# Kernel tuning notes

Hardware: AMD Instinct MI355X
Metric: run time of the kernel (lower is better)

Reference implementation:

```python
import jax, jax.numpy as jnp
import numpy as np

D_MODEL = 1024
NUM_HEADS = 16
D_K = D_MODEL // NUM_HEADS
BATCH = 4
SEQ = 2048


def setup_inputs() -> dict:
    key = jax.random.key(0)
    ks = jax.random.split(key, 16)
    s = 0.02
    return {
        "query": jax.random.normal(ks[0], (BATCH, SEQ, D_MODEL), jnp.float32),
        "key": jax.random.normal(ks[1], (BATCH, SEQ, D_MODEL), jnp.float32),
        "value": jax.random.normal(ks[2], (BATCH, SEQ, D_MODEL), jnp.float32),
        "Wq": jax.random.normal(ks[3], (D_MODEL, D_MODEL), jnp.float32) * s,
        "bq": jnp.zeros((D_MODEL,), jnp.float32),
        "Wk": jax.random.normal(ks[4], (D_MODEL, D_MODEL), jnp.float32) * s,
        "bk": jnp.zeros((D_MODEL,), jnp.float32),
        "Wv": jax.random.normal(ks[5], (D_MODEL, D_MODEL), jnp.float32) * s,
        "bv": jnp.zeros((D_MODEL,), jnp.float32),
        "Wo": jax.random.normal(ks[6], (D_MODEL, D_MODEL), jnp.float32) * s,
        "bo": jnp.zeros((D_MODEL,), jnp.float32),
        "gamma": jnp.ones((D_MODEL,), jnp.float32),
        "beta": jnp.zeros((D_MODEL,), jnp.float32),
    }


def _layer_norm(x, gamma, beta, eps=1e-5):
    mu = jnp.mean(x, axis=-1, keepdims=True)
    var = jnp.var(x, axis=-1, keepdims=True)
    return (x - mu) * jax.lax.rsqrt(var + eps) * gamma + beta


def reference(query, key, value, Wq, bq, Wk, bk, Wv, bv, Wo, bo, gamma, beta):
    B, S, _ = query.shape
    residual = query
    # projections -> [B, H, S, d_k]
    Q = (query @ Wq + bq).reshape(B, S, NUM_HEADS, D_K).transpose(0, 2, 1, 3)
    K = (key @ Wk + bk).reshape(B, -1, NUM_HEADS, D_K).transpose(0, 2, 1, 3)
    V = (value @ Wv + bv).reshape(B, -1, NUM_HEADS, D_K).transpose(0, 2, 1, 3)
    scale = 1.0 / jnp.sqrt(jnp.asarray(D_K, query.dtype))
    scores = jnp.einsum("bhqd,bhkd->bhqk", Q, K) * scale  # [B,H,S,S]
    attn = jax.nn.softmax(scores, axis=-1)
    ctx = jnp.einsum("bhqk,bhkd->bhqd", attn, V)
    ctx = ctx.transpose(0, 2, 1, 3).reshape(B, S, D_MODEL)
    out = ctx @ Wo + bo
    return _layer_norm(residual + out, gamma, beta)
```

## Files before the change

kernel.cpp:

```cpp
#include <hip/hip_runtime.h>

#define D_MODEL 1024
#define NUM_HEADS 16
#define DK 64
#define BATCH 4
#define SEQ 2048
#define MTOT (BATCH*SEQ)

typedef __attribute__((ext_vector_type(8))) short short8;
typedef __attribute__((ext_vector_type(4))) float f32x4;

__device__ __forceinline__ unsigned short f2bf(float f) {
    union { float f; unsigned u; } v; v.f = f;
    unsigned r = v.u + 0x7FFFu + ((v.u >> 16) & 1u);
    return (unsigned short)(r >> 16);
}

__device__ __forceinline__ void gload16(const unsigned short* g, unsigned short* l) {
    __builtin_amdgcn_global_load_lds(
        (const __attribute__((address_space(1))) unsigned int*)g,
        (__attribute__((address_space(3))) unsigned int*)l, 16, 0, 0);
}

__global__ __launch_bounds__(256) void mha_wtrans4(
    const float* __restrict__ W0, const float* __restrict__ W1,
    const float* __restrict__ W2, const float* __restrict__ W3,
    unsigned short* __restrict__ T0, unsigned short* __restrict__ T1,
    unsigned short* __restrict__ T2, unsigned short* __restrict__ T3) {
    __shared__ float tile[64][65];
    int z = blockIdx.z;
    const float* W = z == 0 ? W0 : z == 1 ? W1 : z == 2 ? W2 : W3;
    unsigned short* WT = z == 0 ? T0 : z == 1 ? T1 : z == 2 ? T2 : T3;
    int n0 = blockIdx.x * 64, k0 = blockIdx.y * 64;
    int tx = threadIdx.x & 63, ty = threadIdx.x >> 6;
#pragma unroll
    for (int i = 0; i < 16; ++i)
        tile[ty + i * 4][tx] = W[(size_t)(k0 + ty + i * 4) * D_MODEL + n0 + tx];
    __syncthreads();
#pragma unroll
    for (int i = 0; i < 16; ++i)
        WT[(size_t)(n0 + ty + i * 4) * D_MODEL + k0 + tx] = f2bf(tile[tx][ty + i * 4]);
}

__global__ __launch_bounds__(256) void mha_cvt3(
    const float* __restrict__ i0, const float* __restrict__ i1, const float* __restrict__ i2,
    unsigned short* __restrict__ o0, unsigned short* __restrict__ o1, unsigned short* __restrict__ o2) {
    int y = blockIdx.y;
    const float* in = y == 0 ? i0 : y == 1 ? i1 : i2;
    unsigned short* out = y == 0 ? o0 : y == 1 ? o1 : o2;
    int i = blockIdx.x * 256 + threadIdx.x;
    float4 v = reinterpret_cast<const float4*>(in)[i];
    ushort4 o;
    o.x = f2bf(v.x); o.y = f2bf(v.y); o.z = f2bf(v.z); o.w = f2bf(v.w);
    reinterpret_cast<ushort4*>(out)[i] = o;
}

__device__ __forceinline__ void gemm_stage(const unsigned short* Ag, const unsigned short* Bg,
                                           unsigned short* Al, unsigned short* Bl,
                                           int wid, int rsub, int c8, int kk,
                                           int brow, int bcol) {
#pragma unroll
    for (int q = 0; q < 4; ++q) {
        int i = wid * 4 + q;
        int row = i * 8 + rsub;
        int gcol = kk + ((c8 ^ (row & 7)) << 3);
        gload16(Ag + (size_t)(brow + row) * D_MODEL + gcol, Al + i * 512);
        gload16(Bg + (size_t)(bcol + row) * D_MODEL + gcol, Bl + i * 512);
    }
}

__device__ __forceinline__ void gemm_compute(const unsigned short* Al, const unsigned short* Bl,
                                             f32x4 (&acc)[4][4],
                                             int wr, int wc, int l15, int lg, int l7) {
    short8 af[4][2], bf[4][2];
#pragma unroll
    for (int mi = 0; mi < 4; ++mi)
#pragma unroll
        for (int ks = 0; ks < 2; ++ks)
            af[mi][ks] = *reinterpret_cast<const short8*>(
                &Al[(wr * 64 + mi * 16 + l15) * 64 + (((ks * 4 + lg) ^ l7) << 3)]);
#pragma unroll
    for (int ni = 0; ni < 4; ++ni)
#pragma unroll
        for (int ks = 0; ks < 2; ++ks)
            bf[ni][ks] = *reinterpret_cast<const short8*>(
                &Bl[(wc * 64 + ni * 16 + l15) * 64 + (((ks * 4 + lg) ^ l7) << 3)]);
#pragma unroll
    for (int mi = 0; mi < 4; ++mi)
#pragma unroll
        for (int ni = 0; ni < 4; ++ni)
#pragma unroll
            for (int ks = 0; ks < 2; ++ks)
                acc[mi][ni] = __builtin_amdgcn_mfma_f32_16x16x32_bf16(
                    af[mi][ks], bf[ni][ks], acc[mi][ni], 0, 0, 0);
}

__global__ __launch_bounds__(256) void mha_gemm_qkv(
    const unsigned short* __restrict__ Aq, const unsigned short* __restrict__ Ak,
    const unsigned short* __restrict__ Av,
    const unsigned short* __restrict__ Wq, const unsigned short* __restrict__ Wk,
    const unsigned short* __restrict__ Wv,
    const float* __restrict__ bq, const float* __restrict__ bk, const float* __restrict__ bv,
    unsigned short* __restrict__ Qb, unsigned short* __restrict__ Kb,
    unsigned short* __restrict__ VT, float qscale) {
    __shared__ unsigned short SM[32768];
    unsigned short* A0 = SM;
    unsigned short* B0 = SM + 8192;
    unsigned short* A1 = SM + 16384;
    unsigned short* B1 = SM + 24576;

    int z = blockIdx.z;
    const unsigned short* A = z == 0 ? Aq : z == 1 ? Ak : Av;
    const unsigned short* WT = z == 0 ? Wq : z == 1 ? Wk : Wv;
    const float* bias = z == 0 ? bq : z == 1 ? bk : bv;

    int wid = threadIdx.x >> 6;
    int lane = threadIdx.x & 63;
    int wr = wid >> 1, wc = wid & 1;
    int brow = blockIdx.x * 128;
    int bcol = blockIdx.y * 128;
    int l15 = lane & 15, lg = lane >> 4;
    int c8 = lane & 7, rsub = lane >> 3;
    int l7 = l15 & 7;

    f32x4 acc[4][4] = {};
    gemm_stage(A, WT, A0, B0, wid, rsub, c8, 0, brow, bcol);
    __syncthreads();
    for (int kk = 0; kk < D_MODEL; kk += 128) {
        gemm_stage(A, WT, A1, B1, wid, rsub, c8, kk + 64, brow, bcol);
        gemm_compute(A0, B0, acc, wr, wc, l15, lg, l7);
        __syncthreads();
        if (kk + 128 < D_MODEL)
            gemm_stage(A, WT, A0, B0, wid, rsub, c8, kk + 128, brow, bcol);
        gemm_compute(A1, B1, acc, wr, wc, l15, lg, l7);
        __syncthreads();
    }

    if (z < 2) {
        unsigned short* outb = z == 0 ? Qb : Kb;
        float scale = z == 0 ? qscale : 1.0f;
#pragma unroll
        for (int ni = 0; ni < 4; ++ni) {
            int col = bcol + wc * 64 + ni * 16 + l15;
            float bv2 = bias[col];
#pragma unroll
            for (int mi = 0; mi < 4; ++mi)
#pragma unroll
                for (int j = 0; j < 4; ++j) {
                    int row = brow + wr * 64 + mi * 16 + lg * 4 + j;
                    outb[(size_t)row * D_MODEL + col] = f2bf((acc[mi][ni][j] + bv2) * scale);
                }
        }
    } else {
        unsigned short* T = SM;
#pragma unroll
        for (int ni = 0; ni < 4; ++ni) {
            int c = wc * 64 + ni * 16 + l15;
            float bv2 = bias[bcol + c];
#pragma unroll
            for (int mi = 0; mi < 4; ++mi)
#pragma unroll
                for (int j = 0; j < 4; ++j) {
                    int r = wr * 64 + mi * 16 + lg * 4 + j;
                    T[c * 136 + r] = f2bf(acc[mi][ni][j] + bv2);
                }
        }
        __syncthreads();
        int c = threadIdx.x >> 1;
        int rh = (threadIdx.x & 1) * 64;
        int gcol = bcol + c;
        int h = gcol >> 6, d = gcol & 63;
        int b = brow >> 11, s0 = brow & (SEQ - 1);
        unsigned short* dst = VT + ((size_t)((b * 16 + h) * 64 + d)) * SEQ + s0 + rh;
        const unsigned short* src = &T[c * 136 + rh];
#pragma unroll
        for (int i = 0; i < 8; ++i)
            *reinterpret_cast<short8*>(dst + i * 8) =
                *reinterpret_cast<const short8*>(src + i * 8);
    }
}

__global__ __launch_bounds__(256) void mha_gemm_o(const unsigned short* __restrict__ A,
                                                  const unsigned short* __restrict__ WT,
                                                  const float* __restrict__ bias,
                                                  const float* __restrict__ residual,
                                                  float* __restrict__ outf) {
    __shared__ unsigned short SM[32768];
    unsigned short* A0 = SM;
    unsigned short* B0 = SM + 8192;
    unsigned short* A1 = SM + 16384;
    unsigned short* B1 = SM + 24576;

    int wid = threadIdx.x >> 6;
    int lane = threadIdx.x & 63;
    int wr = wid >> 1, wc = wid & 1;
    int brow = blockIdx.x * 128;
    int bcol = blockIdx.y * 128;
    int l15 = lane & 15, lg = lane >> 4;
    int c8 = lane & 7, rsub = lane >> 3;
    int l7 = l15 & 7;

    f32x4 acc[4][4] = {};
    gemm_stage(A, WT, A0, B0, wid, rsub, c8, 0, brow, bcol);
    __syncthreads();
    for (int kk = 0; kk < D_MODEL; kk += 128) {
        gemm_stage(A, WT, A1, B1, wid, rsub, c8, kk + 64, brow, bcol);
        gemm_compute(A0, B0, acc, wr, wc, l15, lg, l7);
        __syncthreads();
        if (kk + 128 < D_MODEL)
            gemm_stage(A, WT, A0, B0, wid, rsub, c8, kk + 128, brow, bcol);
        gemm_compute(A1, B1, acc, wr, wc, l15, lg, l7);
        __syncthreads();
    }
#pragma unroll
    for (int ni = 0; ni < 4; ++ni) {
        int col = bcol + wc * 64 + ni * 16 + l15;
        float bv2 = bias[col];
#pragma unroll
        for (int mi = 0; mi < 4; ++mi)
#pragma unroll
            for (int j = 0; j < 4; ++j) {
                int row = brow + wr * 64 + mi * 16 + lg * 4 + j;
                outf[(size_t)row * D_MODEL + col] =
                    acc[mi][ni][j] + bv2 + residual[(size_t)row * D_MODEL + col];
            }
    }
}

__device__ __forceinline__ void attn_tile(const unsigned short* Kd,
                                          const unsigned short* Vd,
                                          unsigned short* const* pc,
                                          const unsigned short* Pw,
                                          const short8 aq[2][2],
                                          f32x4 (&acc)[2][4],
                                          float (&lsum)[2][4],
                                          int l15, int lg, int l7) {
    f32x4 s[2][4];
#pragma unroll
    for (int t = 0; t < 4; ++t) {
        int krow = (t * 16 + l15) * 64;
        short8 kf0 = *reinterpret_cast<const short8*>(&Kd[krow + ((lg ^ l7) << 3)]);
        short8 kf1 = *reinterpret_cast<const short8*>(&Kd[krow + (((4 + lg) ^ l7) << 3)]);
#pragma unroll
        for (int m = 0; m < 2; ++m) {
            f32x4 z = {};
            z = __builtin_amdgcn_mfma_f32_16x16x32_bf16(aq[m][0], kf0, z, 0, 0, 0);
            z = __builtin_amdgcn_mfma_f32_16x16x32_bf16(aq[m][1], kf1, z, 0, 0, 0);
            s[m][t] = z;
        }
    }
#pragma unroll
    for (int m = 0; m < 2; ++m)
#pragma unroll
        for (int t = 0; t < 4; ++t)
#pragma unroll
            for (int j = 0; j < 4; ++j) {
                float p = __builtin_amdgcn_exp2f(s[m][t][j]);
                lsum[m][j] += p;
                unsigned u = __builtin_bit_cast(unsigned, p);
                pc[(j & 1) | ((t ^ (j >> 1)) << 1)][m * 1024 + j * 64] =
                    (unsigned short)(u >> 16);
            }
    short8 pf[2][2];
#pragma unroll
    for (int m = 0; m < 2; ++m) {
        int prow = (m * 16 + l15) * 64;
#pragma unroll
        for (int ks = 0; ks < 2; ++ks)
            pf[m][ks] = *reinterpret_cast<const short8*>(
                &Pw[prow + (((ks * 4 + lg) ^ l7) << 3)]);
    }
#pragma unroll
    for (int t = 0; t < 4; ++t) {
        int vrow = (t * 16 + l15) * 64;
        short8 vf0 = *reinterpret_cast<const short8*>(&Vd[vrow + ((lg ^ l7) << 3)]);
        short8 vf1 = *reinterpret_cast<const short8*>(&Vd[vrow + (((4 + lg) ^ l7) << 3)]);
#pragma unroll
        for (int m = 0; m < 2; ++m) {
            acc[m][t] = __builtin_amdgcn_mfma_f32_16x16x32_bf16(pf[m][0], vf0, acc[m][t], 0, 0, 0);
            acc[m][t] = __builtin_amdgcn_mfma_f32_16x16x32_bf16(pf[m][1], vf1, acc[m][t], 0, 0, 0);
        }
    }
}

__global__ __launch_bounds__(256) void mha_attn(const unsigned short* __restrict__ Q,
                                                const unsigned short* __restrict__ K,
                                                const unsigned short* __restrict__ VT,
                                                unsigned short* __restrict__ ctx) {
    __shared__ unsigned short K0[64 * 64], V0[64 * 64];
    __shared__ unsigned short K1[64 * 64], V1[64 * 64];
    __shared__ unsigned short P_lds[4][32 * 64];

    int lane = threadIdx.x & 63;
    int w = threadIdx.x >> 6;
    int l15 = lane & 15, lg = lane >> 4;
    int l7 = l15 & 7;
    int c8 = lane & 7, rsub = lane >> 3;

    int id = blockIdx.x + gridDim.x * blockIdx.y;
    int nid = (id & 7) * 128 + (id >> 3);
    int bx = nid & 15;
    int bh = nid >> 4;
    int b = bh >> 4, h = bh & 15;
    int q0 = bx * 128 + w * 32;

    unsigned short* Pw = P_lds[w];
    unsigned short* pc[8];
    {
        unsigned Bl = lg * 256 + l15 + ((lg & 1) << 5);
#pragma unroll
        for (int c = 0; c < 8; ++c) pc[c] = Pw + (Bl ^ (c << 3));
    }

    short8 aq[2][2];
    {
        const unsigned short* Qp = Q + (size_t)(b * SEQ + q0) * D_MODEL + h * DK;
#pragma unroll
        for (int m = 0; m < 2; ++m)
#pragma unroll
            for (int ks = 0; ks < 2; ++ks)
                aq[m][ks] = *reinterpret_cast<const short8*>(
                    Qp + (size_t)(m * 16 + l15) * D_MODEL + ks * 32 + lg * 8);
    }

    f32x4 acc[2][4] = {};
    float lsum[2][4] = {};

    const unsigned short* Kbh = K + (size_t)(b * SEQ) * D_MODEL + h * DK;
    const unsigned short* VTbh = VT + (size_t)bh * DK * SEQ;

    int i0 = w * 2, i1 = w * 2 + 1;
    int row0 = i0 * 8 + rsub, row1 = i1 * 8 + rsub;
    int sw0 = (c8 ^ (row0 & 7)) << 3, sw1 = (c8 ^ (row1 & 7)) << 3;

#define STAGE(Kd, Vd, kb)                                                        \
    do {                                                                         \
        gload16(Kbh + (size_t)((kb) + row0) * D_MODEL + sw0, (Kd) + i0 * 512);   \
        gload16(Kbh + (size_t)((kb) + row1) * D_MODEL + sw1, (Kd) + i1 * 512);   \
        gload16(VTbh + (size_t)row0 * SEQ + (kb) + sw0, (Vd) + i0 * 512);        \
        gload16(VTbh + (size_t)row1 * SEQ + (kb) + sw1, (Vd) + i1 * 512);        \
    } while (0)

    STAGE(K0, V0, 0);
    __syncthreads();

    for (int kb = 0; kb < SEQ; kb += 128) {
        STAGE(K1, V1, kb + 64);
        attn_tile(K0, V0, pc, Pw, aq, acc, lsum, l15, lg, l7);
        __syncthreads();
        if (kb + 128 < SEQ) STAGE(K0, V0, kb + 128);
        attn_tile(K1, V1, pc, Pw, aq, acc, lsum, l15, lg, l7);
        __syncthreads();
    }
#undef STAGE

#pragma unroll
    for (int m = 0; m < 2; ++m)
#pragma unroll
        for (int j = 0; j < 4; ++j) {
            float l = lsum[m][j];
            l += __shfl_xor(l, 1);
            l += __shfl_xor(l, 2);
            l += __shfl_xor(l, 4);
            l += __shfl_xor(l, 8);
            lsum[m][j] = 1.0f / l;
        }
#pragma unroll
    for (int m = 0; m < 2; ++m)
#pragma unroll
        for (int t = 0; t < 4; ++t)
#pragma unroll
            for (int j = 0; j < 4; ++j) {
                int row = q0 + m * 16 + lg * 4 + j;
                ctx[(size_t)(b * SEQ + row) * D_MODEL + h * DK + t * 16 + l15] =
                    f2bf(acc[m][t][j] * lsum[m][j]);
            }
}

__global__ __launch_bounds__(256) void mha_ln(const float* __restrict__ X,
                                              const float* __restrict__ gamma,
                                              const float* __restrict__ beta,
                                              float* __restrict__ out) {
    int row = blockIdx.x;
    int t = threadIdx.x;
    const float* x = X + (size_t)row * D_MODEL;
    float4 v = reinterpret_cast<const float4*>(x)[t];
    float s = v.x + v.y + v.z + v.w;
    float s2 = v.x * v.x + v.y * v.y + v.z * v.z + v.w * v.w;
#pragma unroll
    for (int off = 1; off < 64; off <<= 1) {
        s += __shfl_xor(s, off);
        s2 += __shfl_xor(s2, off);
    }
    __shared__ float ws[8];
    int wid = t >> 6;
    if ((t & 63) == 0) { ws[wid] = s; ws[4 + wid] = s2; }
    __syncthreads();
    s = ws[0] + ws[1] + ws[2] + ws[3];
    s2 = ws[4] + ws[5] + ws[6] + ws[7];
    float mu = s * (1.f / D_MODEL);
    float var = s2 * (1.f / D_MODEL) - mu * mu;
    float rstd = rsqrtf(var + 1e-5f);
    float4 gv = reinterpret_cast<const float4*>(gamma)[t];
    float4 bv = reinterpret_cast<const float4*>(beta)[t];
    float4 o;
    o.x = (v.x - mu) * rstd * gv.x + bv.x;
    o.y = (v.y - mu) * rstd * gv.y + bv.y;
    o.z = (v.z - mu) * rstd * gv.z + bv.z;
    o.w = (v.w - mu) * rstd * gv.w + bv.w;
    reinterpret_cast<float4*>(out + (size_t)row * D_MODEL)[t] = o;
}

extern "C" void kernel_launch(void* const* d_in, const int* in_sizes, int n_in,
                              void* d_out, int out_size, void* d_ws, size_t ws_size,
                              hipStream_t stream) {
    const float* query = (const float*)d_in[0];
    const float* key   = (const float*)d_in[1];
    const float* value = (const float*)d_in[2];
    const float* Wq = (const float*)d_in[3];
    const float* bq = (const float*)d_in[4];
    const float* Wk = (const float*)d_in[5];
    const float* bk = (const float*)d_in[6];
    const float* Wv = (const float*)d_in[7];
    const float* bv = (const float*)d_in[8];
    const float* Wo = (const float*)d_in[9];
    const float* bo = (const float*)d_in[10];
    const float* gamma = (const float*)d_in[11];
    const float* beta  = (const float*)d_in[12];

    char* ws = (char*)d_ws;
    const size_t MB = 1u << 20;
    unsigned short* WTq = (unsigned short*)(ws + 0 * MB);
    unsigned short* WTk = (unsigned short*)(ws + 2 * MB);
    unsigned short* WTv = (unsigned short*)(ws + 4 * MB);
    unsigned short* WTo = (unsigned short*)(ws + 6 * MB);
    unsigned short* Aq  = (unsigned short*)(ws + 8 * MB);
    unsigned short* Ak  = (unsigned short*)(ws + 24 * MB);
    unsigned short* Av  = (unsigned short*)(ws + 40 * MB);
    unsigned short* Qb  = (unsigned short*)(ws + 56 * MB);
    unsigned short* Kb  = (unsigned short*)(ws + 72 * MB);
    unsigned short* VT  = (unsigned short*)(ws + 88 * MB);
    unsigned short* ctx = (unsigned short*)(ws + 92 * MB);
    float* tmp          = (float*)(ws + 24 * MB);

    const float C1 = 0.180336880f;

    dim3 b256(256);
    mha_wtrans4<<<dim3(16, 16, 4), b256, 0, stream>>>(Wq, Wk, Wv, Wo, WTq, WTk, WTv, WTo);

    int nblk = (MTOT * D_MODEL / 4) / 256;
    mha_cvt3<<<dim3(nblk, 3), b256, 0, stream>>>(query, key, value, Aq, Ak, Av);

    mha_gemm_qkv<<<dim3(MTOT / 128, D_MODEL / 128, 3), b256, 0, stream>>>(
        Aq, Ak, Av, WTq, WTk, WTv, bq, bk, bv, Qb, Kb, VT, C1);

    mha_attn<<<dim3(SEQ / 128, BATCH * NUM_HEADS), b256, 0, stream>>>(Qb, Kb, VT, ctx);

    mha_gemm_o<<<dim3(MTOT / 128, D_MODEL / 128), b256, 0, stream>>>(ctx, WTo, bo, query, tmp);

    mha_ln<<<dim3(MTOT), b256, 0, stream>>>(tmp, gamma, beta, (float*)d_out);
}
```

Baseline: 230.6 us.

## Keep attention probabilities in registers by computing transposed scores

Swaps the MFMA operand order so S^T is computed, letting the exp'd probabilities be packed straight into bf16 B-operand fragments with v_cvt_pk_bf16_f32 instead of round-tripping through a per-wave LDS P buffer. The K rows loaded into LDS are permuted so the accumulator layout matches the operand layout expected by the PV MFMA. Row sums now need only two cross-lane shuffles, output stores become 8-byte vectors, and the removal of the P buffer plus launch_bounds(256,4) aims for higher occupancy. P is now rounded to bf16 (round-to-nearest) rather than truncated, and the row permutation must be exactly right for correctness.

```diff
diff --git a/kernel.cpp b/kernel.cpp
--- a/kernel.cpp
+++ b/kernel.cpp
@@ -9,11 +9,18 @@
 
 typedef __attribute__((ext_vector_type(8))) short short8;
 typedef __attribute__((ext_vector_type(4))) float f32x4;
+typedef __attribute__((ext_vector_type(4))) unsigned int u32x4;
 
 __device__ __forceinline__ unsigned short f2bf(float f) {
     union { float f; unsigned u; } v; v.f = f;
     unsigned r = v.u + 0x7FFFu + ((v.u >> 16) & 1u);
     return (unsigned short)(r >> 16);
+}
+
+__device__ __forceinline__ unsigned cvtpk(float lo, float hi) {
+    unsigned r;
+    asm("v_cvt_pk_bf16_f32 %0, %1, %2" : "=v"(r) : "v"(lo), "v"(hi));
+    return r;
 }
 
 __device__ __forceinline__ void gload16(const unsigned short* g, unsigned short* l) {
@@ -229,13 +236,11 @@
 
 __device__ __forceinline__ void attn_tile(const unsigned short* Kd,
                                           const unsigned short* Vd,
-                                          unsigned short* const* pc,
-                                          const unsigned short* Pw,
                                           const short8 aq[2][2],
                                           f32x4 (&acc)[2][4],
-                                          float (&lsum)[2][4],
+                                          float (&lsum)[2],
                                           int l15, int lg, int l7) {
-    f32x4 s[2][4];
+    f32x4 z[2][4];
 #pragma unroll
     for (int t = 0; t < 4; ++t) {
         int krow = (t * 16 + l15) * 64;
@@ -243,10 +248,10 @@
         short8 kf1 = *reinterpret_cast<const short8*>(&Kd[krow + (((4 + lg) ^ l7) << 3)]);
 #pragma unroll
         for (int m = 0; m < 2; ++m) {
-            f32x4 z = {};
-            z = __builtin_amdgcn_mfma_f32_16x16x32_bf16(aq[m][0], kf0, z, 0, 0, 0);
-            z = __builtin_amdgcn_mfma_f32_16x16x32_bf16(aq[m][1], kf1, z, 0, 0, 0);
-            s[m][t] = z;
+            f32x4 zz = {};
+            zz = __builtin_amdgcn_mfma_f32_16x16x32_bf16(kf0, aq[m][0], zz, 0, 0, 0);
+            zz = __builtin_amdgcn_mfma_f32_16x16x32_bf16(kf1, aq[m][1], zz, 0, 0, 0);
+            z[m][t] = zz;
         }
     }
 #pragma unroll
@@ -255,41 +260,41 @@
         for (int t = 0; t < 4; ++t)
 #pragma unroll
             for (int j = 0; j < 4; ++j) {
-                float p = __builtin_amdgcn_exp2f(s[m][t][j]);
-                lsum[m][j] += p;
-                unsigned u = __builtin_bit_cast(unsigned, p);
-                pc[(j & 1) | ((t ^ (j >> 1)) << 1)][m * 1024 + j * 64] =
-                    (unsigned short)(u >> 16);
+                float p = __builtin_amdgcn_exp2f(z[m][t][j]);
+                z[m][t][j] = p;
+                lsum[m] += p;
             }
     short8 pf[2][2];
 #pragma unroll
-    for (int m = 0; m < 2; ++m) {
-        int prow = (m * 16 + l15) * 64;
-#pragma unroll
-        for (int ks = 0; ks < 2; ++ks)
-            pf[m][ks] = *reinterpret_cast<const short8*>(
-                &Pw[prow + (((ks * 4 + lg) ^ l7) << 3)]);
-    }
-#pragma unroll
-    for (int t = 0; t < 4; ++t) {
-        int vrow = (t * 16 + l15) * 64;
+    for (int m = 0; m < 2; ++m)
+#pragma unroll
+        for (int ks = 0; ks < 2; ++ks) {
+            union { u32x4 u; short8 s; } cv;
+            cv.u = (u32x4){cvtpk(z[m][2 * ks][0], z[m][2 * ks][1]),
+                           cvtpk(z[m][2 * ks][2], z[m][2 * ks][3]),
+                           cvtpk(z[m][2 * ks + 1][0], z[m][2 * ks + 1][1]),
+                           cvtpk(z[m][2 * ks + 1][2], z[m][2 * ks + 1][3])};
+            pf[m][ks] = cv.s;
+        }
+#pragma unroll
+    for (int dt = 0; dt < 4; ++dt) {
+        int vrow = (dt * 16 + l15) * 64;
         short8 vf0 = *reinterpret_cast<const short8*>(&Vd[vrow + ((lg ^ l7) << 3)]);
         short8 vf1 = *reinterpret_cast<const short8*>(&Vd[vrow + (((4 + lg) ^ l7) << 3)]);
 #pragma unroll
         for (int m = 0; m < 2; ++m) {
-            acc[m][t] = __builtin_amdgcn_mfma_f32_16x16x32_bf16(pf[m][0], vf0, acc[m][t], 0, 0, 0);
-            acc[m][t] = __builtin_amdgcn_mfma_f32_16x16x32_bf16(pf[m][1], vf1, acc[m][t], 0, 0, 0);
-        }
-    }
-}
-
-__global__ __launch_bounds__(256) void mha_attn(const unsigned short* __restrict__ Q,
-                                                const unsigned short* __restrict__ K,
-                                                const unsigned short* __restrict__ VT,
-                                                unsigned short* __restrict__ ctx) {
+            acc[m][dt] = __builtin_amdgcn_mfma_f32_16x16x32_bf16(vf0, pf[m][0], acc[m][dt], 0, 0, 0);
+            acc[m][dt] = __builtin_amdgcn_mfma_f32_16x16x32_bf16(vf1, pf[m][1], acc[m][dt], 0, 0, 0);
+        }
+    }
+}
+
+__global__ __launch_bounds__(256, 4) void mha_attn(const unsigned short* __restrict__ Q,
+                                                   const unsigned short* __restrict__ K,
+                                                   const unsigned short* __restrict__ VT,
+                                                   unsigned short* __restrict__ ctx) {
     __shared__ unsigned short K0[64 * 64], V0[64 * 64];
     __shared__ unsigned short K1[64 * 64], V1[64 * 64];
-    __shared__ unsigned short P_lds[4][32 * 64];
 
     int lane = threadIdx.x & 63;
     int w = threadIdx.x >> 6;
@@ -304,14 +309,6 @@
     int b = bh >> 4, h = bh & 15;
     int q0 = bx * 128 + w * 32;
 
-    unsigned short* Pw = P_lds[w];
-    unsigned short* pc[8];
-    {
-        unsigned Bl = lg * 256 + l15 + ((lg & 1) << 5);
-#pragma unroll
-        for (int c = 0; c < 8; ++c) pc[c] = Pw + (Bl ^ (c << 3));
-    }
-
     short8 aq[2][2];
     {
         const unsigned short* Qp = Q + (size_t)(b * SEQ + q0) * D_MODEL + h * DK;
@@ -324,7 +321,7 @@
     }
 
     f32x4 acc[2][4] = {};
-    float lsum[2][4] = {};
+    float lsum[2] = {};
 
     const unsigned short* Kbh = K + (size_t)(b * SEQ) * D_MODEL + h * DK;
     const unsigned short* VTbh = VT + (size_t)bh * DK * SEQ;
@@ -332,11 +329,13 @@
     int i0 = w * 2, i1 = w * 2 + 1;
     int row0 = i0 * 8 + rsub, row1 = i1 * 8 + rsub;
     int sw0 = (c8 ^ (row0 & 7)) << 3, sw1 = (c8 ^ (row1 & 7)) << 3;
+    int sr0 = (row0 & 32) | ((row0 & 12) << 1) | ((row0 & 16) >> 2) | (row0 & 3);
+    int sr1 = (row1 & 32) | ((row1 & 12) << 1) | ((row1 & 16) >> 2) | (row1 & 3);
 
 #define STAGE(Kd, Vd, kb)                                                        \
     do {                                                                         \
-        gload16(Kbh + (size_t)((kb) + row0) * D_MODEL + sw0, (Kd) + i0 * 512);   \
-        gload16(Kbh + (size_t)((kb) + row1) * D_MODEL + sw1, (Kd) + i1 * 512);   \
+        gload16(Kbh + (size_t)((kb) + sr0) * D_MODEL + sw0, (Kd) + i0 * 512);    \
+        gload16(Kbh + (size_t)((kb) + sr1) * D_MODEL + sw1, (Kd) + i1 * 512);    \
         gload16(VTbh + (size_t)row0 * SEQ + (kb) + sw0, (Vd) + i0 * 512);        \
         gload16(VTbh + (size_t)row1 * SEQ + (kb) + sw1, (Vd) + i1 * 512);        \
     } while (0)
@@ -346,35 +345,32 @@
 
     for (int kb = 0; kb < SEQ; kb += 128) {
         STAGE(K1, V1, kb + 64);
-        attn_tile(K0, V0, pc, Pw, aq, acc, lsum, l15, lg, l7);
+        attn_tile(K0, V0, aq, acc, lsum, l15, lg, l7);
         __syncthreads();
         if (kb + 128 < SEQ) STAGE(K0, V0, kb + 128);
-        attn_tile(K1, V1, pc, Pw, aq, acc, lsum, l15, lg, l7);
+        attn_tile(K1, V1, aq, acc, lsum, l15, lg, l7);
         __syncthreads();
     }
 #undef STAGE
 
 #pragma unroll
-    for (int m = 0; m < 2; ++m)
-#pragma unroll
-        for (int j = 0; j < 4; ++j) {
-            float l = lsum[m][j];
-            l += __shfl_xor(l, 1);
-            l += __shfl_xor(l, 2);
-            l += __shfl_xor(l, 4);
-            l += __shfl_xor(l, 8);
-            lsum[m][j] = 1.0f / l;
-        }
-#pragma unroll
-    for (int m = 0; m < 2; ++m)
-#pragma unroll
-        for (int t = 0; t < 4; ++t)
-#pragma unroll
-            for (int j = 0; j < 4; ++j) {
-                int row = q0 + m * 16 + lg * 4 + j;
-                ctx[(size_t)(b * SEQ + row) * D_MODEL + h * DK + t * 16 + l15] =
-                    f2bf(acc[m][t][j] * lsum[m][j]);
-            }
+    for (int m = 0; m < 2; ++m) {
+        float l = lsum[m];
+        l += __shfl_xor(l, 16);
+        l += __shfl_xor(l, 32);
+        float rl = 1.0f / l;
+        int q = q0 + m * 16 + l15;
+        unsigned short* cp = ctx + (size_t)(b * SEQ + q) * D_MODEL + h * DK + lg * 4;
+#pragma unroll
+        for (int dt = 0; dt < 4; ++dt) {
+            ushort4 o;
+            o.x = f2bf(acc[m][dt][0] * rl);
+            o.y = f2bf(acc[m][dt][1] * rl);
+            o.z = f2bf(acc[m][dt][2] * rl);
+            o.w = f2bf(acc[m][dt][3] * rl);
+            *reinterpret_cast<ushort4*>(cp + dt * 16) = o;
+        }
+    }
 }
 
 __global__ __launch_bounds__(256) void mha_ln(const float* __restrict__ X,
```

Measured after the change: 200.2 us. -13.2%, faster.
